# Kernel optimization log

Measured on AMD Instinct MI355X. Metric: run time of the kernel, lower is better.

The kernel has to match this reference:

```python
import jax, jax.numpy as jnp
import numpy as np

B = 16384

def _linear_params(key, out_dim, in_dim):
    k1, k2 = jax.random.split(key)
    s = 1.0 / np.sqrt(in_dim)
    W = jax.random.uniform(k1, (out_dim, in_dim), jnp.float32, -s, s)
    b = jax.random.uniform(k2, (out_dim,), jnp.float32, -s, s)
    return W, b

def setup_inputs() -> dict:
    key = jax.random.key(0)
    ks = jax.random.split(key, 6)
    x = jax.random.normal(ks[0], (B, 784), jnp.float32)
    conv_w = jax.random.normal(ks[1], (3, 3), jnp.float32)
    W1, b1 = _linear_params(ks[2], 1024, 26 * 26)
    W2, b2 = _linear_params(ks[3], 512, 1024)
    W3, b3 = _linear_params(ks[4], 256, 512)
    W4, b4 = _linear_params(ks[5], 10, 256)
    return {"x": x, "conv_w": conv_w, "W1": W1, "b1": b1, "W2": W2, "b2": b2,
            "W3": W3, "b3": b3, "W4": W4, "b4": b4}

def reference(x, conv_w, W1, b1, W2, b2, W3, b3, W4, b4):
    b = x.shape[0]
    img = x.reshape(b, 1, 28, 28)                       # NCHW
    kern = conv_w.reshape(1, 1, 3, 3)                   # OIHW; cross-correlation
    y = jax.lax.conv_general_dilated(img, kern, (1, 1), 'VALID')  # [B,1,26,26]
    h = y.reshape(b, 26 * 26)
    h = jax.nn.relu(h @ W1.T + b1)
    h = jax.nn.relu(h @ W2.T + b2)
    h = jax.nn.relu(h @ W3.T + b3)
    return h @ W4.T + b4                                # [B,10] logits
```

## Files before the change

### kernel.cpp

```cpp
#include <hip/hip_runtime.h>
#include <hip/hip_bf16.h>
#include <stdint.h>

#define BDIM 256

typedef __attribute__((ext_vector_type(8))) short short8;
typedef __attribute__((ext_vector_type(4))) float f32x4;
typedef __attribute__((ext_vector_type(4))) unsigned int u32x4;

__device__ __forceinline__ unsigned short f2bf(float f) {
  union { float f; unsigned u; } v; v.f = f;
  unsigned r = v.u + 0x7fffu + ((v.u >> 16) & 1u);
  return (unsigned short)(r >> 16);
}
__device__ __forceinline__ float bf2f(unsigned short u) {
  union { unsigned u; float f; } v; v.u = ((unsigned)u) << 16;
  return v.f;
}

__global__ __launch_bounds__(BDIM) void cast_pad_w1(const float* __restrict__ w,
                                                    unsigned short* __restrict__ o) {
  int idx = blockIdx.x * BDIM + threadIdx.x;
  if (idx >= 1024 * 704) return;
  int n = idx / 704, k = idx - n * 704;
  float v = (k < 676) ? w[n * 676 + k] : 0.f;
  o[idx] = f2bf(v);
}

__global__ __launch_bounds__(BDIM) void cast_plain(const float* __restrict__ w,
                                                   unsigned short* __restrict__ o, int count) {
  int idx = blockIdx.x * BDIM + threadIdx.x;
  if (idx < count) o[idx] = f2bf(w[idx]);
}

__global__ __launch_bounds__(BDIM) void conv3x3(const float* __restrict__ x,
                                                const float* __restrict__ cw,
                                                unsigned short* __restrict__ h0) {
  __shared__ float xs[784];
  __shared__ float w[9];
  int m = blockIdx.x;
  const float* xr = x + (size_t)m * 784;
  if (threadIdx.x < 9) w[threadIdx.x] = cw[threadIdx.x];
  for (int i = threadIdx.x; i < 784; i += BDIM) xs[i] = xr[i];
  __syncthreads();
  unsigned short* hr = h0 + (size_t)m * 704;
  for (int p = threadIdx.x; p < 704; p += BDIM) {
    float v = 0.f;
    if (p < 676) {
      int r = p / 26, c = p - r * 26;
      const float* xp = &xs[r * 28 + c];
      v = xp[0]  * w[0] + xp[1]  * w[1] + xp[2]  * w[2]
        + xp[28] * w[3] + xp[29] * w[4] + xp[30] * w[5]
        + xp[56] * w[6] + xp[57] * w[7] + xp[58] * w[8];
    }
    hr[p] = f2bf(v);
  }
}

template <bool RELU>
__global__ __launch_bounds__(BDIM) void gemm_bt(const unsigned short* __restrict__ A,
                                                const unsigned short* __restrict__ Wt,
                                                const float* __restrict__ bias,
                                                unsigned short* __restrict__ Cb,
                                                int M, int N, int K) {
  __shared__ unsigned short As[128 * 32];
  __shared__ unsigned short Bs[128 * 32];
  const int tid = threadIdx.x;
  const int lane = tid & 63;
  const int wid = tid >> 6;
  const int nbm = M >> 7;
  const int brow = (blockIdx.x % nbm) << 7;
  const int bcol = (blockIdx.x / nbm) << 7;

  const int r0 = tid >> 2;
  const int c0 = (tid & 3) * 8;
  const int r1 = r0 + 64;
  const unsigned short* gA0 = A + (size_t)(brow + r0) * K + c0;
  const unsigned short* gA1 = A + (size_t)(brow + r1) * K + c0;
  const unsigned short* gB0 = Wt + (size_t)(bcol + r0) * K + c0;
  const unsigned short* gB1 = Wt + (size_t)(bcol + r1) * K + c0;
  unsigned short* sA0 = As + tid * 8;
  unsigned short* sA1 = As + 2048 + tid * 8;
  unsigned short* sB0 = Bs + tid * 8;
  unsigned short* sB1 = Bs + 2048 + tid * 8;

  u32x4 ra0 = *(const u32x4*)gA0, ra1 = *(const u32x4*)gA1;
  u32x4 rb0 = *(const u32x4*)gB0, rb1 = *(const u32x4*)gB1;

  f32x4 acc[4][4] = {};

  const int wr = (wid >> 1) << 6;
  const int wc = (wid & 1) << 6;
  const int fr = lane & 15;
  const int fk = (lane >> 4) << 3;
  const unsigned short* pa = As + (wr + fr) * 32 + fk;
  const unsigned short* pb = Bs + (wc + fr) * 32 + fk;

  const int nk = K >> 5;
  for (int kt = 0; kt < nk; ++kt) {
    __syncthreads();
    *(u32x4*)sA0 = ra0; *(u32x4*)sA1 = ra1;
    *(u32x4*)sB0 = rb0; *(u32x4*)sB1 = rb1;
    __syncthreads();
    if (kt + 1 < nk) {
      gA0 += 32; gA1 += 32; gB0 += 32; gB1 += 32;
      ra0 = *(const u32x4*)gA0; ra1 = *(const u32x4*)gA1;
      rb0 = *(const u32x4*)gB0; rb1 = *(const u32x4*)gB1;
    }
    short8 af[4], bf[4];
#pragma unroll
    for (int m = 0; m < 4; ++m) af[m] = *(const short8*)(pa + m * 512);
#pragma unroll
    for (int n = 0; n < 4; ++n) bf[n] = *(const short8*)(pb + n * 512);
#pragma unroll
    for (int m = 0; m < 4; ++m)
#pragma unroll
      for (int n = 0; n < 4; ++n)
        acc[m][n] = __builtin_amdgcn_mfma_f32_16x16x32_bf16(af[m], bf[n], acc[m][n], 0, 0, 0);
  }

  const int crow = brow + wr + ((lane >> 4) << 2);
  const int ccol0 = bcol + wc + (lane & 15);
#pragma unroll
  for (int n = 0; n < 4; ++n) {
    const int cc = ccol0 + n * 16;
    const float bv = bias[cc];
#pragma unroll
    for (int m = 0; m < 4; ++m) {
      const int rr = crow + m * 16;
#pragma unroll
      for (int j = 0; j < 4; ++j) {
        float v = acc[m][n][j] + bv;
        if (RELU) v = v > 0.f ? v : 0.f;
        Cb[(size_t)(rr + j) * N + cc] = f2bf(v);
      }
    }
  }
}

__global__ __launch_bounds__(BDIM) void fc10(const unsigned short* __restrict__ h3,
                                             const float* __restrict__ W4,
                                             const float* __restrict__ b4,
                                             float* __restrict__ out) {
  int lane = threadIdx.x & 63;
  int wid = threadIdx.x >> 6;
  int m = blockIdx.x * 4 + wid;
  const unsigned short* hr = h3 + (size_t)m * 256 + lane * 4;
  uint64_t hv = *(const uint64_t*)hr;
  float e0 = bf2f((unsigned short)hv), e1 = bf2f((unsigned short)(hv >> 16));
  float e2 = bf2f((unsigned short)(hv >> 32)), e3 = bf2f((unsigned short)(hv >> 48));
#pragma unroll
  for (int n = 0; n < 10; ++n) {
    const float4 wv = *(const float4*)(W4 + n * 256 + lane * 4);
    float s = e0 * wv.x + e1 * wv.y + e2 * wv.z + e3 * wv.w;
#pragma unroll
    for (int off = 32; off > 0; off >>= 1) s += __shfl_xor(s, off);
    if (lane == n) out[(size_t)m * 10 + n] = s + b4[n];
  }
}

extern "C" void kernel_launch(void* const* d_in, const int* in_sizes, int n_in,
                              void* d_out, int out_size, void* d_ws, size_t ws_size,
                              hipStream_t stream) {
  const float* x  = (const float*)d_in[0];
  const float* cw = (const float*)d_in[1];
  const float* W1 = (const float*)d_in[2];
  const float* b1 = (const float*)d_in[3];
  const float* W2 = (const float*)d_in[4];
  const float* b2 = (const float*)d_in[5];
  const float* W3 = (const float*)d_in[6];
  const float* b3 = (const float*)d_in[7];
  const float* W4 = (const float*)d_in[8];
  const float* b4 = (const float*)d_in[9];
  float* out = (float*)d_out;

  char* ws = (char*)d_ws;
  unsigned short* h0  = (unsigned short*)(ws);
  unsigned short* h1  = (unsigned short*)(ws + 23068672);
  unsigned short* W1b = (unsigned short*)(ws + 23068672 + 33554432);
  unsigned short* W2b = W1b + 1024 * 704;
  unsigned short* W3b = W2b + 512 * 1024;
  unsigned short* h2  = h0;
  unsigned short* h3  = h1;

  cast_pad_w1<<<2816, BDIM, 0, stream>>>(W1, W1b);
  cast_plain<<<2048, BDIM, 0, stream>>>(W2, W2b, 512 * 1024);
  cast_plain<<<512, BDIM, 0, stream>>>(W3, W3b, 256 * 512);
  conv3x3<<<16384, BDIM, 0, stream>>>(x, cw, h0);

  gemm_bt<true><<<(16384 / 128) * (1024 / 128), BDIM, 0, stream>>>(h0, W1b, b1, h1, 16384, 1024, 704);
  gemm_bt<true><<<(16384 / 128) * (512 / 128),  BDIM, 0, stream>>>(h1, W2b, b2, h2, 16384, 512, 1024);
  gemm_bt<true><<<(16384 / 128) * (256 / 128),  BDIM, 0, stream>>>(h2, W3b, b3, h3, 16384, 256, 512);
  fc10<<<16384 / 4, BDIM, 0, stream>>>(h3, W4, b4, out);
}
```

Before: 123.2 us.

## Use direct global-to-LDS loads with double-buffered shared tiles in GEMM

```diff
diff --git a/kernel.cpp b/kernel.cpp
--- a/kernel.cpp
+++ b/kernel.cpp
@@ -6,7 +6,10 @@
 
 typedef __attribute__((ext_vector_type(8))) short short8;
 typedef __attribute__((ext_vector_type(4))) float f32x4;
-typedef __attribute__((ext_vector_type(4))) unsigned int u32x4;
+
+#define AS1 __attribute__((address_space(1)))
+#define AS3 __attribute__((address_space(3)))
+#define GLL16(g, s) __builtin_amdgcn_global_load_lds((AS1 const void*)(g), (AS3 void*)(s), 16, 0, 0)
 
 __device__ __forceinline__ unsigned short f2bf(float f) {
   union { float f; unsigned u; } v; v.f = f;
@@ -63,8 +66,8 @@
                                                 const float* __restrict__ bias,
                                                 unsigned short* __restrict__ Cb,
                                                 int M, int N, int K) {
-  __shared__ unsigned short As[128 * 32];
-  __shared__ unsigned short Bs[128 * 32];
+  __shared__ unsigned short As[2][128 * 32];
+  __shared__ unsigned short Bs[2][128 * 32];
   const int tid = threadIdx.x;
   const int lane = tid & 63;
   const int wid = tid >> 6;
@@ -72,20 +75,21 @@
   const int brow = (blockIdx.x % nbm) << 7;
   const int bcol = (blockIdx.x / nbm) << 7;
 
-  const int r0 = tid >> 2;
-  const int c0 = (tid & 3) * 8;
-  const int r1 = r0 + 64;
-  const unsigned short* gA0 = A + (size_t)(brow + r0) * K + c0;
-  const unsigned short* gA1 = A + (size_t)(brow + r1) * K + c0;
-  const unsigned short* gB0 = Wt + (size_t)(bcol + r0) * K + c0;
-  const unsigned short* gB1 = Wt + (size_t)(bcol + r1) * K + c0;
-  unsigned short* sA0 = As + tid * 8;
-  unsigned short* sA1 = As + 2048 + tid * 8;
-  unsigned short* sB0 = Bs + tid * 8;
-  unsigned short* sB1 = Bs + 2048 + tid * 8;
+  const int srow = (wid << 4) + (lane >> 2);
+  const int scol = (lane & 3) << 3;
+  const unsigned short* gA0 = A + (size_t)(brow + srow) * K + scol;
+  const unsigned short* gA1 = A + (size_t)(brow + 64 + srow) * K + scol;
+  const unsigned short* gB0 = Wt + (size_t)(bcol + srow) * K + scol;
+  const unsigned short* gB1 = Wt + (size_t)(bcol + 64 + srow) * K + scol;
+  const int ldsoff = wid << 9;
 
-  u32x4 ra0 = *(const u32x4*)gA0, ra1 = *(const u32x4*)gA1;
-  u32x4 rb0 = *(const u32x4*)gB0, rb1 = *(const u32x4*)gB1;
+#define STAGE(buf, koff)                                   \
+  do {                                                     \
+    GLL16(gA0 + (koff), &As[buf][ldsoff]);                 \
+    GLL16(gA1 + (koff), &As[buf][2048 + ldsoff]);          \
+    GLL16(gB0 + (koff), &Bs[buf][ldsoff]);                 \
+    GLL16(gB1 + (koff), &Bs[buf][2048 + ldsoff]);          \
+  } while (0)
 
   f32x4 acc[4][4] = {};
 
@@ -93,20 +97,17 @@
   const int wc = (wid & 1) << 6;
   const int fr = lane & 15;
   const int fk = (lane >> 4) << 3;
-  const unsigned short* pa = As + (wr + fr) * 32 + fk;
-  const unsigned short* pb = Bs + (wc + fr) * 32 + fk;
+  const int aoff = (wr + fr) * 32 + fk;
+  const int boff = (wc + fr) * 32 + fk;
 
   const int nk = K >> 5;
+  STAGE(0, 0);
+  __syncthreads();
+  int cur = 0;
   for (int kt = 0; kt < nk; ++kt) {
-    __syncthreads();
-    *(u32x4*)sA0 = ra0; *(u32x4*)sA1 = ra1;
-    *(u32x4*)sB0 = rb0; *(u32x4*)sB1 = rb1;
-    __syncthreads();
-    if (kt + 1 < nk) {
-      gA0 += 32; gA1 += 32; gB0 += 32; gB1 += 32;
-      ra0 = *(const u32x4*)gA0; ra1 = *(const u32x4*)gA1;
-      rb0 = *(const u32x4*)gB0; rb1 = *(const u32x4*)gB1;
-    }
+    if (kt + 1 < nk) STAGE(cur ^ 1, (kt + 1) * 32);
+    const unsigned short* pa = &As[cur][aoff];
+    const unsigned short* pb = &Bs[cur][boff];
     short8 af[4], bf[4];
 #pragma unroll
     for (int m = 0; m < 4; ++m) af[m] = *(const short8*)(pa + m * 512);
@@ -117,7 +118,10 @@
 #pragma unroll
       for (int n = 0; n < 4; ++n)
         acc[m][n] = __builtin_amdgcn_mfma_f32_16x16x32_bf16(af[m], bf[n], acc[m][n], 0, 0, 0);
+    __syncthreads();
+    cur ^= 1;
   }
+#undef STAGE
 
   const int crow = brow + wr + ((lane >> 4) << 2);
   const int ccol0 = bcol + wc + (lane & 15);
```

Result: slower. 131.9 us (+7.1%).
